# Kernel tuning notes

Hardware: AMD Instinct MI355X
Metric: run time of the kernel (lower is better)

Reference implementation:

```python
import jax, jax.numpy as jnp
import numpy as np

B, S, D, H, DFF, K = 16, 1024, 1024, 16, 4096, 3


def setup_inputs() -> dict:
    key = jax.random.key(0)
    ks = jax.random.split(key, 8)
    f = lambda k, sh: jax.random.normal(k, sh, jnp.float32) * 0.02
    return dict(
        x=jax.random.normal(ks[0], (B, S, D), jnp.float32),
        mask=jnp.ones((B, 1, S), jnp.int32),
        alpha1=jnp.ones((D,), jnp.float32), bias1=jnp.zeros((D,), jnp.float32),
        alpha2=jnp.ones((D,), jnp.float32), bias2=jnp.zeros((D,), jnp.float32),
        W_l1=f(ks[1], (D, 2 * D)), b_l1=jnp.zeros((2 * D,), jnp.float32),
        conv_w=f(ks[2], (H, K)),
        W_l2=f(ks[3], (D, D)), b_l2=jnp.zeros((D,), jnp.float32),
        W_ff1=f(ks[4], (D, DFF)), b_ff1=jnp.zeros((DFF,), jnp.float32),
        W_ff2=f(ks[5], (DFF, D)), b_ff2=jnp.zeros((D,), jnp.float32),
    )


def _norm(x, alpha, bias, eps=1e-6):
    # Norm: alpha * (x - mean) / (std + eps) + bias, torch std is unbiased (ddof=1)
    mu = x.mean(-1, keepdims=True)
    sd = x.std(-1, keepdims=True, ddof=1)
    return alpha * (x - mu) / (sd + eps) + bias


def _lightconv(x, conv_w):
    # x: [B, S, C]; conv_w: [H, K] softmax-normalized over K; channels in a head share kernel
    C = x.shape[-1]
    w = jax.nn.softmax(conv_w, axis=-1)              # [H, K]
    wk = jnp.repeat(w, C // H, axis=0)[:, None, :]   # [C, 1, K] depthwise kernel
    y = jax.lax.conv_general_dilated(
        x.transpose(0, 2, 1), wk, (1,), [(K // 2, (K - 1) // 2)],
        dimension_numbers=('NCH', 'OIH', 'NCH'), feature_group_count=C)
    return y.transpose(0, 2, 1)


def reference(x, mask, alpha1, bias1, alpha2, bias2, W_l1, b_l1, conv_w,
              W_l2, b_l2, W_ff1, b_ff1, W_ff2, b_ff2):
    # --- lightweight-conv sublayer ---
    res = x
    h = _norm(x, alpha1, bias1)
    h = h @ W_l1 + b_l1                         # [B,S,2C]
    a, b = jnp.split(h, 2, axis=-1)
    h = a * jax.nn.sigmoid(b)                   # GLU -> [B,S,C]
    cm = mask[:, -1, :][:, :, None]             # [B,S,1]
    h = jnp.where(cm == 0, 0.0, h)
    h = _lightconv(h, conv_w)
    h = h @ W_l2 + b_l2
    x = res + h
    # --- FFN sublayer ---
    res = x
    h = _norm(x, alpha2, bias2)
    h = jax.nn.relu(h @ W_ff1 + b_ff1) @ W_ff2 + b_ff2
    return res + h
```

## Files before the change

### kernel.cpp

```cpp
#include <hip/hip_runtime.h>

typedef unsigned short ushort_t;
typedef __attribute__((ext_vector_type(8))) short s8v;
typedef __attribute__((ext_vector_type(4))) float f4v;

__device__ __forceinline__ float b2f(ushort_t h) {
    union { unsigned u; float f; } c; c.u = ((unsigned)h) << 16; return c.f;
}
__device__ __forceinline__ ushort_t f2b(float f) {
    union { float f; unsigned u; } c; c.f = f;
    unsigned u = c.u;
    return (ushort_t)((u + 0x7fffu + ((u >> 16) & 1u)) >> 16);
}

__device__ __forceinline__ void glds16(const void* g, void* l) {
    __builtin_amdgcn_global_load_lds(
        (const __attribute__((address_space(1))) void*)g,
        (__attribute__((address_space(3))) void*)l, 16, 0, 0);
}

__global__ __launch_bounds__(256) void trans_k(const float* __restrict__ W,
                                               ushort_t* __restrict__ Wt,
                                               int K, int N) {
    __shared__ float tile[64][65];
    int k0 = blockIdx.x * 64, n0 = blockIdx.y * 64;
    int t = threadIdx.x;
    int c = t & 63, r4 = t >> 6;
#pragma unroll
    for (int i = 0; i < 16; ++i) {
        int r = i * 4 + r4;
        tile[r][c] = W[(size_t)(k0 + r) * N + n0 + c];
    }
    __syncthreads();
#pragma unroll
    for (int i = 0; i < 16; ++i) {
        int r = i * 4 + r4;
        Wt[(size_t)(n0 + r) * K + k0 + c] = f2b(tile[c][r]);
    }
}

__global__ __launch_bounds__(256) void norm_k(const float* __restrict__ x,
                                              const float* __restrict__ al,
                                              const float* __restrict__ be,
                                              ushort_t* __restrict__ out) {
    int row = blockIdx.x;
    const float4* xr = (const float4*)(x + (size_t)row * 1024);
    float4 v = xr[threadIdx.x];
    float s = v.x + v.y + v.z + v.w;
    float q = v.x * v.x + v.y * v.y + v.z * v.z + v.w * v.w;
#pragma unroll
    for (int o = 32; o > 0; o >>= 1) {
        s += __shfl_down(s, o);
        q += __shfl_down(q, o);
    }
    __shared__ float ss[4], qq[4];
    int lane = threadIdx.x & 63, wv = threadIdx.x >> 6;
    if (lane == 0) { ss[wv] = s; qq[wv] = q; }
    __syncthreads();
    s = ss[0] + ss[1] + ss[2] + ss[3];
    q = qq[0] + qq[1] + qq[2] + qq[3];
    float mu = s * (1.f / 1024.f);
    float var = (q - 1024.f * mu * mu) * (1.f / 1023.f);
    var = fmaxf(var, 0.f);
    float inv = 1.f / (sqrtf(var) + 1e-6f);
    float4 a4 = ((const float4*)al)[threadIdx.x];
    float4 b4 = ((const float4*)be)[threadIdx.x];
    ushort4 o4;
    o4.x = f2b(a4.x * (v.x - mu) * inv + b4.x);
    o4.y = f2b(a4.y * (v.y - mu) * inv + b4.y);
    o4.z = f2b(a4.z * (v.z - mu) * inv + b4.z);
    o4.w = f2b(a4.w * (v.w - mu) * inv + b4.w);
    ((ushort4*)(out + (size_t)row * 1024))[threadIdx.x] = o4;
}

__global__ __launch_bounds__(256) void glu_k(const ushort_t* __restrict__ t1,
                                             const int* __restrict__ mask,
                                             ushort_t* __restrict__ g) {
    int i = blockIdx.x * 256 + threadIdx.x;
    int row = i >> 7;
    int cc = (i & 127) << 3;
    int b = row >> 10, s = row & 1023;
    size_t base = (size_t)row * 2048;
    s8v va = *(const s8v*)(t1 + base + cc);
    s8v vb = *(const s8v*)(t1 + base + 1024 + cc);
    float mval = (mask[b * 1024 + s] == 0) ? 0.f : 1.f;
    s8v ov;
#pragma unroll
    for (int j = 0; j < 8; ++j) {
        float a = b2f((ushort_t)va[j]);
        float xx = b2f((ushort_t)vb[j]);
        float sg = 1.f / (1.f + __expf(-xx));
        ov[j] = (short)f2b(a * sg * mval);
    }
    *(s8v*)(g + (size_t)row * 1024 + cc) = ov;
}

__global__ __launch_bounds__(256) void conv_k(const ushort_t* __restrict__ g,
                                              const float* __restrict__ cw,
                                              ushort_t* __restrict__ out) {
    int i = blockIdx.x * 256 + threadIdx.x;
    int row = i >> 7;
    int cc = (i & 127) << 3;
    int s = row & 1023;
    int head = cc >> 6;
    float w0 = cw[head * 3 + 0], w1 = cw[head * 3 + 1], w2 = cw[head * 3 + 2];
    float mx = fmaxf(w0, fmaxf(w1, w2));
    float e0 = __expf(w0 - mx), e1 = __expf(w1 - mx), e2 = __expf(w2 - mx);
    float inv = 1.f / (e0 + e1 + e2);
    w0 = e0 * inv; w1 = e1 * inv; w2 = e2 * inv;
    size_t base = (size_t)row * 1024 + cc;
    s8v z = {0, 0, 0, 0, 0, 0, 0, 0};
    s8v vm = (s > 0)    ? *(const s8v*)(g + base - 1024) : z;
    s8v v0 = *(const s8v*)(g + base);
    s8v vp = (s < 1023) ? *(const s8v*)(g + base + 1024) : z;
    s8v ov;
#pragma unroll
    for (int j = 0; j < 8; ++j) {
        float r = w0 * b2f((ushort_t)vm[j]) + w1 * b2f((ushort_t)v0[j]) +
                  w2 * b2f((ushort_t)vp[j]);
        ov[j] = (short)f2b(r);
    }
    *(s8v*)(out + base) = ov;
}

template <int EPI>
__global__ __launch_bounds__(512, 2) void gemm_k(const ushort_t* __restrict__ A,
                                                 const ushort_t* __restrict__ Bt,
                                                 const float* __restrict__ bias,
                                                 const float* res, float* outf,
                                                 ushort_t* outb, int N, int K) {
    __shared__ char smem[131072] __attribute__((aligned(128)));
    const int NBN = N >> 8;
    const int nwg = gridDim.x;
    const int per = nwg >> 3;
    const int tt = (blockIdx.x & 7) * per + (blockIdx.x >> 3);
    const int gw = NBN << 3;
    const int g = tt / gw;
    const int rem = tt - g * gw;
    const int bm = (g << 3) + (rem & 7);
    const int bn = rem >> 3;

    const int t = threadIdx.x;
    const int l = t & 63, w = t >> 6;
    const int wm = w >> 2, wn = w & 3;
    const int lr = l & 15, lk = l >> 4;

    const int swzel = (((t & 3) ^ ((t >> 3) & 3)) << 3);
    const int r0 = t >> 2;
    const ushort_t* pA0 = A + (size_t)(bm * 256 + r0) * K + swzel;
    const ushort_t* pA1 = pA0 + (size_t)128 * K;
    const ushort_t* pB0 = Bt + (size_t)(bn * 256 + r0) * K + swzel;
    const ushort_t* pB1 = pB0 + (size_t)128 * K;

    const int fswz = ((lk ^ ((lr >> 1) & 3)) << 4);
    int aoffL[4], aoffH[4], boff[4];
#pragma unroll
    for (int m = 0; m < 4; ++m) {
        aoffL[m] = (wm * 128 + m * 16 + lr) * 64 + fswz;
        aoffH[m] = (wm * 128 + (4 + m) * 16 + lr) * 64 + fswz;
        boff[m] = 16384 + (wn * 64 + m * 16 + lr) * 64 + fswz;
    }

    f4v acc[8][4];
#pragma unroll
    for (int m = 0; m < 8; ++m)
#pragma unroll
        for (int n = 0; n < 4; ++n) acc[m][n] = f4v{0.f, 0.f, 0.f, 0.f};

    const int NK = K >> 5;

#pragma unroll
    for (int p = 0; p < 3; ++p) {
        char* d = smem + p * 32768 + t * 16;
        glds16(pA0 + p * 32, d);
        glds16(pA1 + p * 32, d + 8192);
        glds16(pB0 + p * 32, d + 16384);
        glds16(pB1 + p * 32, d + 24576);
    }
    asm volatile("s_waitcnt vmcnt(8)" ::: "memory");
    __builtin_amdgcn_sched_barrier(0);
    __builtin_amdgcn_s_barrier();

    s8v aL0[4], bC0[4], aL1[4], bC1[4], aH[4];
#pragma unroll
    for (int m = 0; m < 4; ++m) aL0[m] = *(const s8v*)(smem + aoffL[m]);
#pragma unroll
    for (int n = 0; n < 4; ++n) bC0[n] = *(const s8v*)(smem + boff[n]);

#define KSTEP(I, CAL, CB, NAL, NB)                                             \
    {                                                                          \
        const int i_ = (I);                                                    \
        const char* cb_ = smem + (size_t)(i_ & 3) * 32768;                     \
        const int nx_ = (i_ + 1 < NK) ? i_ + 1 : NK - 1;                       \
        const char* nb_ = smem + (size_t)(nx_ & 3) * 32768;                    \
        int st_ = i_ + 3; if (st_ >= NK) st_ = NK - 1;                         \
        char* sd_ = smem + (size_t)((i_ + 3) & 3) * 32768 + t * 16;            \
        const int ko_ = st_ * 32;                                              \
                                                             \
        _Pragma("unroll")                                                      \
        for (int m = 0; m < 4; ++m) aH[m] = *(const s8v*)(cb_ + aoffH[m]);     \
        glds16(pA0 + ko_, sd_);                                                \
        glds16(pA1 + ko_, sd_ + 8192);                                         \
        asm volatile("s_waitcnt vmcnt(6)" ::: "memory");                       \
        __builtin_amdgcn_sched_barrier(0);                                     \
        __builtin_amdgcn_s_barrier();                                          \
        asm volatile("s_waitcnt lgkmcnt(4)" ::: "memory");                     \
        __builtin_amdgcn_sched_barrier(0);                                     \
        __builtin_amdgcn_s_setprio(1);                                         \
        _Pragma("unroll")                                                      \
        for (int m = 0; m < 4; ++m)                                            \
            _Pragma("unroll")                                                  \
            for (int n = 0; n < 4; ++n)                                        \
                acc[m][n] = __builtin_amdgcn_mfma_f32_16x16x32_bf16(           \
                    CAL[m], CB[n], acc[m][n], 0, 0, 0);                        \
        __builtin_amdgcn_s_setprio(0);                                         \
        __builtin_amdgcn_sched_barrier(0);                                     \
        __builtin_amdgcn_s_barrier();                                          \
                                                             \
        _Pragma("unroll")                                                      \
        for (int m = 0; m < 4; ++m) NAL[m] = *(const s8v*)(nb_ + aoffL[m]);    \
        _Pragma("unroll")                                                      \
        for (int n = 0; n < 4; ++n) NB[n] = *(const s8v*)(nb_ + boff[n]);      \
        glds16(pB0 + ko_, sd_ + 16384);                                        \
        glds16(pB1 + ko_, sd_ + 24576);                                        \
        __builtin_amdgcn_s_barrier();                                          \
        asm volatile("s_waitcnt lgkmcnt(8)" ::: "memory");                     \
        __builtin_amdgcn_sched_barrier(0);                                     \
        __builtin_amdgcn_s_setprio(1);                                         \
        _Pragma("unroll")                                                      \
        for (int m = 0; m < 4; ++m)                                            \
            _Pragma("unroll")                                                  \
            for (int n = 0; n < 4; ++n)                                        \
                acc[4 + m][n] = __builtin_amdgcn_mfma_f32_16x16x32_bf16(       \
                    aH[m], CB[n], acc[4 + m][n], 0, 0, 0);                     \
        __builtin_amdgcn_s_setprio(0);                                         \
        __builtin_amdgcn_sched_barrier(0);                                     \
        __builtin_amdgcn_s_barrier();                                          \
    }

    for (int ii = 0; ii < NK; ii += 2) {
        KSTEP(ii, aL0, bC0, aL1, bC1);
        KSTEP(ii + 1, aL1, bC1, aL0, bC0);
    }
#undef KSTEP

    if (EPI == 1) {
#pragma unroll
        for (int n = 0; n < 4; ++n) {
            int gcol = bn * 256 + wn * 64 + n * 16 + lr;
            float bb = bias[gcol];
#pragma unroll
            for (int m = 0; m < 8; ++m) {
#pragma unroll
                for (int r = 0; r < 4; ++r) {
                    int grow = bm * 256 + wm * 128 + m * 16 + lk * 4 + r;
                    size_t oi = (size_t)grow * N + gcol;
                    outf[oi] = acc[m][n][r] + bb + res[oi];
                }
            }
        }
    } else {
        asm volatile("s_waitcnt vmcnt(0)" ::: "memory");
        __builtin_amdgcn_s_barrier();
        float biasr[4];
#pragma unroll
        for (int n = 0; n < 4; ++n)
            biasr[n] = bias[bn * 256 + wn * 64 + n * 16 + lr];
        char* sB = smem;
#pragma unroll
        for (int half = 0; half < 2; ++half) {
#pragma unroll
            for (int m4 = 0; m4 < 4; ++m4)
#pragma unroll
                for (int n = 0; n < 4; ++n)
#pragma unroll
                    for (int r = 0; r < 4; ++r) {
                        int rl = wm * 64 + m4 * 16 + lk * 4 + r;
                        int cl = wn * 64 + n * 16 + lr;
                        float v = acc[half * 4 + m4][n][r] + biasr[n];
                        if (EPI == 2) v = fmaxf(v, 0.f);
                        int byt = rl * 512 + ((cl * 2) ^ ((rl & 3) << 4));
                        *(ushort_t*)(sB + byt) = f2b(v);
                    }
            __builtin_amdgcn_s_barrier();
#pragma unroll
            for (int s = 0; s < 8; ++s) {
                int rl = s * 16 + (t >> 5);
                int byt = rl * 512 + (((t & 31) * 16) ^ ((rl & 3) << 4));
                int grow = bm * 256 + (rl >> 6) * 128 + half * 64 + (rl & 63);
                int gcol = bn * 256 + (t & 31) * 8;
                *(s8v*)(outb + (size_t)grow * N + gcol) = *(const s8v*)(sB + byt);
            }
            __builtin_amdgcn_s_barrier();
        }
    }
}

extern "C" void kernel_launch(void* const* d_in, const int* in_sizes, int n_in,
                              void* d_out, int out_size, void* d_ws, size_t ws_size,
                              hipStream_t stream) {
    const float* x      = (const float*)d_in[0];
    const int*   mask   = (const int*)d_in[1];
    const float* alpha1 = (const float*)d_in[2];
    const float* bias1  = (const float*)d_in[3];
    const float* alpha2 = (const float*)d_in[4];
    const float* bias2  = (const float*)d_in[5];
    const float* W_l1   = (const float*)d_in[6];
    const float* b_l1   = (const float*)d_in[7];
    const float* conv_w = (const float*)d_in[8];
    const float* W_l2   = (const float*)d_in[9];
    const float* b_l2   = (const float*)d_in[10];
    const float* W_ff1  = (const float*)d_in[11];
    const float* b_ff1  = (const float*)d_in[12];
    const float* W_ff2  = (const float*)d_in[13];
    const float* b_ff2  = (const float*)d_in[14];
    float* out = (float*)d_out;

    char* ws = (char*)d_ws;
    size_t off = 0;
    auto alloc = [&](size_t b) {
        char* p = ws + off;
        off += (b + 255) & ~(size_t)255;
        return p;
    };
    ushort_t* Wl1t  = (ushort_t*)alloc(2048ull * 1024 * 2);
    ushort_t* Wl2t  = (ushort_t*)alloc(1024ull * 1024 * 2);
    ushort_t* Wff1t = (ushort_t*)alloc(4096ull * 1024 * 2);
    ushort_t* Wff2t = (ushort_t*)alloc(1024ull * 4096 * 2);
    char* regA = alloc(134217728ull);
    ushort_t* B1 = (ushort_t*)alloc(33554432ull);
    ushort_t* C1 = (ushort_t*)alloc(33554432ull);
    ushort_t* t1 = (ushort_t*)regA;
    ushort_t* f1 = (ushort_t*)regA;

    const int R = 16384;

    trans_k<<<dim3(16, 32), 256, 0, stream>>>(W_l1, Wl1t, 1024, 2048);
    trans_k<<<dim3(16, 16), 256, 0, stream>>>(W_l2, Wl2t, 1024, 1024);
    trans_k<<<dim3(16, 64), 256, 0, stream>>>(W_ff1, Wff1t, 1024, 4096);
    trans_k<<<dim3(64, 16), 256, 0, stream>>>(W_ff2, Wff2t, 4096, 1024);

    norm_k<<<R, 256, 0, stream>>>(x, alpha1, bias1, B1);
    gemm_k<0><<<64 * 8, 512, 0, stream>>>(B1, Wl1t, b_l1, nullptr, nullptr, t1, 2048, 1024);
    glu_k<<<8192, 256, 0, stream>>>(t1, mask, B1);
    conv_k<<<8192, 256, 0, stream>>>(B1, conv_w, C1);
    gemm_k<1><<<64 * 4, 512, 0, stream>>>(C1, Wl2t, b_l2, x, out, nullptr, 1024, 1024);

    norm_k<<<R, 256, 0, stream>>>(out, alpha2, bias2, B1);
    gemm_k<2><<<64 * 16, 512, 0, stream>>>(B1, Wff1t, b_ff1, nullptr, nullptr, f1, 4096, 1024);
    gemm_k<1><<<64 * 4, 512, 0, stream>>>(f1, Wff2t, b_ff2, out, out, nullptr, 1024, 4096);
}
```

Before: 575.2 us.

## Restructure GEMM k-loop pipeline with fewer barriers and single-pass epilogue

The GEMM main loop now issues all four global-to-LDS prefetches for stage i+3 at the start of each k-step. It drops the lgkmcnt waits and most of the workgroup barriers, keeping one vmcnt wait plus barrier before the next fragments are read. The goal is less synchronisation stall between the MFMA blocks. Launch bounds move to one block per CU, which the 128KB LDS footprint already forces, so the compiler gets more register room. The bf16 epilogue now stages the whole 256x256 tile through LDS in one pass instead of two halves, at the cost of relying on compiler-inserted LDS waits and on the asm statements no longer having memory clobbers.

```diff
diff --git a/kernel.cpp b/kernel.cpp
--- a/kernel.cpp
+++ b/kernel.cpp
@@ -124,7 +124,7 @@
 }
 
 template <int EPI>
-__global__ __launch_bounds__(512, 2) void gemm_k(const ushort_t* __restrict__ A,
+__global__ __launch_bounds__(512, 1) void gemm_k(const ushort_t* __restrict__ A,
                                                  const ushort_t* __restrict__ Bt,
                                                  const float* __restrict__ bias,
                                                  const float* res, float* outf,
@@ -153,13 +153,13 @@
     const ushort_t* pB1 = pB0 + (size_t)128 * K;
 
     const int fswz = ((lk ^ ((lr >> 1) & 3)) << 4);
-    int aoffL[4], aoffH[4], boff[4];
-#pragma unroll
-    for (int m = 0; m < 4; ++m) {
-        aoffL[m] = (wm * 128 + m * 16 + lr) * 64 + fswz;
-        aoffH[m] = (wm * 128 + (4 + m) * 16 + lr) * 64 + fswz;
-        boff[m] = 16384 + (wn * 64 + m * 16 + lr) * 64 + fswz;
-    }
+    int aoff[8], boff[4];
+#pragma unroll
+    for (int m = 0; m < 8; ++m)
+        aoff[m] = (wm * 128 + m * 16 + lr) * 64 + fswz;
+#pragma unroll
+    for (int n = 0; n < 4; ++n)
+        boff[n] = 16384 + (wn * 64 + n * 16 + lr) * 64 + fswz;
 
     f4v acc[8][4];
 #pragma unroll
@@ -177,70 +177,61 @@
         glds16(pB0 + p * 32, d + 16384);
         glds16(pB1 + p * 32, d + 24576);
     }
-    asm volatile("s_waitcnt vmcnt(8)" ::: "memory");
+    asm volatile("s_waitcnt vmcnt(8)");
+    __builtin_amdgcn_s_barrier();
     __builtin_amdgcn_sched_barrier(0);
-    __builtin_amdgcn_s_barrier();
-
-    s8v aL0[4], bC0[4], aL1[4], bC1[4], aH[4];
-#pragma unroll
-    for (int m = 0; m < 4; ++m) aL0[m] = *(const s8v*)(smem + aoffL[m]);
-#pragma unroll
-    for (int n = 0; n < 4; ++n) bC0[n] = *(const s8v*)(smem + boff[n]);
-
-#define KSTEP(I, CAL, CB, NAL, NB)                                             \
+
+    s8v aL0[4], bF0[4], aL1[4], bF1[4], aH[4];
+#pragma unroll
+    for (int m = 0; m < 4; ++m) aL0[m] = *(const s8v*)(smem + aoff[m]);
+#pragma unroll
+    for (int n = 0; n < 4; ++n) bF0[n] = *(const s8v*)(smem + boff[n]);
+
+#define KSTEP(I, CAL, CBF, NAL, NBF)                                           \
     {                                                                          \
         const int i_ = (I);                                                    \
         const char* cb_ = smem + (size_t)(i_ & 3) * 32768;                     \
-        const int nx_ = (i_ + 1 < NK) ? i_ + 1 : NK - 1;                       \
-        const char* nb_ = smem + (size_t)(nx_ & 3) * 32768;                    \
+        const char* nb_ = smem + (size_t)((i_ + 1) & 3) * 32768;               \
         int st_ = i_ + 3; if (st_ >= NK) st_ = NK - 1;                         \
         char* sd_ = smem + (size_t)((i_ + 3) & 3) * 32768 + t * 16;            \
         const int ko_ = st_ * 32;                                              \
-                                                             \
-        _Pragma("unroll")                                                      \
-        for (int m = 0; m < 4; ++m) aH[m] = *(const s8v*)(cb_ + aoffH[m]);     \
+                 \
+        _Pragma("unroll")                                                      \
+        for (int m = 0; m < 4; ++m) aH[m] = *(const s8v*)(cb_ + aoff[4 + m]);  \
         glds16(pA0 + ko_, sd_);                                                \
         glds16(pA1 + ko_, sd_ + 8192);                                         \
-        asm volatile("s_waitcnt vmcnt(6)" ::: "memory");                       \
-        __builtin_amdgcn_sched_barrier(0);                                     \
-        __builtin_amdgcn_s_barrier();                                          \
-        asm volatile("s_waitcnt lgkmcnt(4)" ::: "memory");                     \
-        __builtin_amdgcn_sched_barrier(0);                                     \
+        glds16(pB0 + ko_, sd_ + 16384);                                        \
+        glds16(pB1 + ko_, sd_ + 24576);                                        \
         __builtin_amdgcn_s_setprio(1);                                         \
         _Pragma("unroll")                                                      \
         for (int m = 0; m < 4; ++m)                                            \
             _Pragma("unroll")                                                  \
             for (int n = 0; n < 4; ++n)                                        \
                 acc[m][n] = __builtin_amdgcn_mfma_f32_16x16x32_bf16(           \
-                    CAL[m], CB[n], acc[m][n], 0, 0, 0);                        \
+                    CAL[m], CBF[n], acc[m][n], 0, 0, 0);                       \
         __builtin_amdgcn_s_setprio(0);                                         \
         __builtin_amdgcn_sched_barrier(0);                                     \
+        asm volatile("s_waitcnt vmcnt(6)");               \
         __builtin_amdgcn_s_barrier();                                          \
-                                                             \
-        _Pragma("unroll")                                                      \
-        for (int m = 0; m < 4; ++m) NAL[m] = *(const s8v*)(nb_ + aoffL[m]);    \
-        _Pragma("unroll")                                                      \
-        for (int n = 0; n < 4; ++n) NB[n] = *(const s8v*)(nb_ + boff[n]);      \
-        glds16(pB0 + ko_, sd_ + 16384);                                        \
-        glds16(pB1 + ko_, sd_ + 24576);                                        \
-        __builtin_amdgcn_s_barrier();                                          \
-        asm volatile("s_waitcnt lgkmcnt(8)" ::: "memory");                     \
         __builtin_amdgcn_sched_barrier(0);                                     \
+           \
+        _Pragma("unroll")                                                      \
+        for (int m = 0; m < 4; ++m) NAL[m] = *(const s8v*)(nb_ + aoff[m]);     \
+        _Pragma("unroll")                                                      \
+        for (int n = 0; n < 4; ++n) NBF[n] = *(const s8v*)(nb_ + boff[n]);     \
         __builtin_amdgcn_s_setprio(1);                                         \
         _Pragma("unroll")                                                      \
         for (int m = 0; m < 4; ++m)                                            \
             _Pragma("unroll")                                                  \
             for (int n = 0; n < 4; ++n)                                        \
                 acc[4 + m][n] = __builtin_amdgcn_mfma_f32_16x16x32_bf16(       \
-                    aH[m], CB[n], acc[4 + m][n], 0, 0, 0);                     \
+                    aH[m], CBF[n], acc[4 + m][n], 0, 0, 0);                    \
         __builtin_amdgcn_s_setprio(0);                                         \
-        __builtin_amdgcn_sched_barrier(0);                                     \
-        __builtin_amdgcn_s_barrier();                                          \
     }
 
     for (int ii = 0; ii < NK; ii += 2) {
-        KSTEP(ii, aL0, bC0, aL1, bC1);
-        KSTEP(ii + 1, aL1, bC1, aL0, bC0);
+        KSTEP(ii, aL0, bF0, aL1, bF1);
+        KSTEP(ii + 1, aL1, bF1, aL0, bF0);
     }
 #undef KSTEP
 
@@ -262,36 +253,30 @@
     } else {
         asm volatile("s_waitcnt vmcnt(0)" ::: "memory");
         __builtin_amdgcn_s_barrier();
-        float biasr[4];
+        float bb4[4];
 #pragma unroll
         for (int n = 0; n < 4; ++n)
-            biasr[n] = bias[bn * 256 + wn * 64 + n * 16 + lr];
-        char* sB = smem;
-#pragma unroll
-        for (int half = 0; half < 2; ++half) {
-#pragma unroll
-            for (int m4 = 0; m4 < 4; ++m4)
-#pragma unroll
-                for (int n = 0; n < 4; ++n)
-#pragma unroll
-                    for (int r = 0; r < 4; ++r) {
-                        int rl = wm * 64 + m4 * 16 + lk * 4 + r;
-                        int cl = wn * 64 + n * 16 + lr;
-                        float v = acc[half * 4 + m4][n][r] + biasr[n];
-                        if (EPI == 2) v = fmaxf(v, 0.f);
-                        int byt = rl * 512 + ((cl * 2) ^ ((rl & 3) << 4));
-                        *(ushort_t*)(sB + byt) = f2b(v);
-                    }
-            __builtin_amdgcn_s_barrier();
-#pragma unroll
-            for (int s = 0; s < 8; ++s) {
-                int rl = s * 16 + (t >> 5);
-                int byt = rl * 512 + (((t & 31) * 16) ^ ((rl & 3) << 4));
-                int grow = bm * 256 + (rl >> 6) * 128 + half * 64 + (rl & 63);
-                int gcol = bn * 256 + (t & 31) * 8;
-                *(s8v*)(outb + (size_t)grow * N + gcol) = *(const s8v*)(sB + byt);
-            }
-            __builtin_amdgcn_s_barrier();
+            bb4[n] = bias[bn * 256 + wn * 64 + n * 16 + lr];
+#pragma unroll
+        for (int m = 0; m < 8; ++m)
+#pragma unroll
+            for (int n = 0; n < 4; ++n)
+#pragma unroll
+                for (int r = 0; r < 4; ++r) {
+                    int row = wm * 128 + m * 16 + lk * 4 + r;
+                    int colb = ((wn * 64 + n * 16 + lr) * 2) ^ ((row & 3) << 4);
+                    float v = acc[m][n][r] + bb4[n];
+                    if (EPI == 2) v = fmaxf(v, 0.f);
+                    *(ushort_t*)(smem + row * 512 + colb) = f2b(v);
+                }
+        __builtin_amdgcn_s_barrier();
+#pragma unroll
+        for (int s = 0; s < 16; ++s) {
+            int row = s * 16 + (t >> 5);
+            int byt = row * 512 + (((t & 31) * 16) ^ ((row & 3) << 4));
+            int grow = bm * 256 + row;
+            int gcol = bn * 256 + (t & 31) * 8;
+            *(s8v*)(outb + (size_t)grow * N + gcol) = *(const s8v*)(smem + byt);
         }
     }
 }
```

Measured after the change: 585.2 us. No clear change (+1.7%).
